# Optimization experiments

Hardware: AMD Instinct MI355X
Metric: run time of the kernel (lower is better)

Reference implementation:

```python
import jax, jax.numpy as jnp
import numpy as np

D_MODEL = 256
D_STATE = 64
R_MIN, R_MAX, MAX_PHASE = 0.0, 1.0, 6.28


def setup_inputs() -> dict:
    key = jax.random.key(0)
    ks = jax.random.split(key, 8)
    u1 = jax.random.uniform(ks[0], (D_STATE,), dtype=jnp.float32)
    u2 = jax.random.uniform(ks[1], (D_STATE,), dtype=jnp.float32)
    nu_log = jnp.log(-0.5 * jnp.log(u1 * (R_MAX**2 - R_MIN**2) + R_MIN**2))
    theta_log = jnp.log(u2 * MAX_PHASE)
    sB = 1.0 / np.sqrt(2 * D_STATE)
    sC = 1.0 / np.sqrt(D_STATE)
    B_re = jax.random.normal(ks[2], (D_MODEL, D_STATE), dtype=jnp.float32) * sB
    B_im = jax.random.normal(ks[3], (D_MODEL, D_STATE), dtype=jnp.float32) * sB
    C_re = jax.random.normal(ks[4], (D_MODEL, D_STATE), dtype=jnp.float32) * sC
    C_im = jax.random.normal(ks[5], (D_MODEL, D_STATE), dtype=jnp.float32) * sC
    D = jax.random.normal(ks[6], (D_MODEL,), dtype=jnp.float32)
    x = jax.random.normal(ks[7], (4, 8192, D_MODEL), dtype=jnp.float32)
    return {"x": x, "nu_log": nu_log, "theta_log": theta_log,
            "B_re": B_re, "B_im": B_im, "C_re": C_re, "C_im": C_im, "D": D}


def reference(x, nu_log, theta_log, B_re, B_im, C_re, C_im, D):
    B, L, H = x.shape
    # diagonal transition: Lambda = exp(-exp(nu) + i*exp(theta)); Lambda^k = exp(k*log_lambda)
    log_lambda = -jnp.exp(nu_log) + 1j * jnp.exp(theta_log)          # (n,)
    k = jnp.arange(L, dtype=jnp.float32)
    Lambda_k = jnp.exp(k[:, None] * log_lambda[None, :])              # (L, n) complex
    CB = (C_re + 1j * C_im) * (B_re + 1j * B_im)                      # (H, n)
    kernels = jnp.einsum('hn,ln->hl', CB, Lambda_k).real              # (H, L)
    # FFT (causal, linear) convolution per channel
    n_fft = 2 * L
    x_f = jnp.fft.rfft(x, n=n_fft, axis=1)                            # (B, L+1, H)
    k_f = jnp.fft.rfft(kernels, n=n_fft, axis=1)                      # (H, L+1)
    y_f = x_f * k_f.T[None]                                           # (B, L+1, H)
    y = jnp.fft.irfft(y_f, n=n_fft, axis=1)[:, :L, :]
    return y + x * D[None, None, :]
```

## Files before the change

### kernel.cpp

```cpp
#include <hip/hip_runtime.h>
#include <hip/hip_bf16.h>

#define BB   4
#define LL   8192
#define HH   256
#define NN   64
#define NSEG 128
#define LSEG 64
#define YCS  258

typedef __attribute__((ext_vector_type(8))) short  short8;
typedef __attribute__((ext_vector_type(4))) float  float4v;
typedef __attribute__((ext_vector_type(4))) int    int4v;


__device__ __forceinline__ float ldF(const void* p, size_t i, int isbf) {
    return isbf ? __bfloat162float(((const __hip_bfloat16*)p)[i])
                : ((const float*)p)[i];
}

__device__ __forceinline__ unsigned int packbf(float re, float im) {
    __hip_bfloat16 hr = __float2bfloat16(re);
    __hip_bfloat16 hi = __float2bfloat16(im);
    return ((unsigned int)*(unsigned short*)&hi << 16)
         |  (unsigned int)*(unsigned short*)&hr;
}
__device__ __forceinline__ float unpkre(unsigned int u) {
    unsigned short s = (unsigned short)(u & 0xFFFFu);
    return __bfloat162float(*(__hip_bfloat16*)&s);
}
__device__ __forceinline__ float unpkim(unsigned int u) {
    unsigned short s = (unsigned short)(u >> 16);
    return __bfloat162float(*(__hip_bfloat16*)&s);
}

__global__ void k_sniff(const void* p0, const void* p1, const void* p2,
                        const void* p3, const void* p4, const void* p5,
                        const void* p6, const void* p7, int* flags)
{
    int t = threadIdx.x;
    if (t < 8) {
        const void* ps[8] = {p0, p1, p2, p3, p4, p5, p6, p7};
        const unsigned int* d = (const unsigned int*)ps[t];
        int nbf = 0, nrand = 0;
        #pragma unroll
        for (int i = 0; i < 32; ++i) {
            unsigned int lo = d[i] & 0xFFFFu;
            unsigned int e  = (lo >> 7) & 0xFFu;
            if (lo == 0u) {  }
            else if (e >= 90u && e <= 140u) nbf++;
            else nrand++;
        }
        flags[t] = (nrand == 0 && nbf >= 8) ? 1 : 0;
    }
}

__global__ __launch_bounds__(256) void k_setup(
    const void* nu_log, const void* theta_log,
    const void* B_re, const void* B_im,
    const void* C_re, const void* C_im,
    const void* D, const int* __restrict__ flags,
    float* lam, float* lam64, float* Df, float* CBt,
    float* PsegRe, float* PsegIm)
{
    int t = blockIdx.x * 256 + threadIdx.x;
    if (t < NN) {
        float nu = expf(ldF(nu_log, t, flags[1]));
        float th = expf(ldF(theta_log, t, flags[2]));
        float a  = expf(-nu);
        lam[2*t]   = a * cosf(th);
        lam[2*t+1] = a * sinf(th);
        float a64 = expf(-64.0f * nu);
        float ph  = 64.0f * th;
        lam64[2*t]   = a64 * cosf(ph);
        lam64[2*t+1] = a64 * sinf(ph);
    }
    if (t < HH) Df[t] = ldF(D, t, flags[7]);
    if (t < HH * NN) {
        int h = t >> 6, n = t & 63;
        float bre = ldF(B_re, h*NN+n, flags[3]);
        float bim = ldF(B_im, h*NN+n, flags[4]);
        float cre = ldF(C_re, h*NN+n, flags[5]);
        float cim = ldF(C_im, h*NN+n, flags[6]);
        CBt[(n*2+0)*HH + h] = cre*bre - cim*bim;
        CBt[(n*2+1)*HH + h] = cre*bim + cim*bre;
    }
    if (t < 64 * 64) {
        int l = t >> 6, n = t & 63;
        float nu = expf(ldF(nu_log, n, flags[1]));
        float th = expf(ldF(theta_log, n, flags[2]));
        float fp = (float)(63 - l);
        float ar = expf(-fp * nu);
        PsegRe[t] = ar * cosf(fp * th);
        PsegIm[t] = ar * sinf(fp * th);
    }
}

__global__ __launch_bounds__(256) void k_ktab(
    const float* __restrict__ CBt, const float* __restrict__ PsegRe,
    const float* __restrict__ PsegIm, const float* __restrict__ lam64,
    float* __restrict__ Ktab,
    short* __restrict__ VreT, short* __restrict__ VimnT,
    short* __restrict__ PreH, short* __restrict__ PreL,
    short* __restrict__ PimH, short* __restrict__ PimL)
{
    int t = blockIdx.x * 256 + threadIdx.x;
    int h = t >> 6, j = t & 63;
    float acc = 0.f;
    for (int n = 0; n < NN; ++n)
        acc += CBt[(2*n)*HH + h]   * PsegRe[(63-j)*64 + n]
             - CBt[(2*n+1)*HH + h] * PsegIm[(63-j)*64 + n];
    Ktab[j*HH + h] = acc;
    if (t < 64*64) {
        int tau = t >> 6, n = t & 63;
        float vr, vi;
        if (tau < 63) {
            vr =  PsegRe[(62-tau)*64 + n];
            vi = -PsegIm[(62-tau)*64 + n];
        } else {
            vr =  lam64[2*n];
            vi = -lam64[2*n+1];
        }
        __hip_bfloat16 br = __float2bfloat16(vr);
        __hip_bfloat16 bi = __float2bfloat16(vi);
        VreT[tau*64 + n]  = *(short*)&br;
        VimnT[tau*64 + n] = *(short*)&bi;

        int n2 = t >> 6, l2 = t & 63;
        float pr = PsegRe[l2*64 + n2];
        float pi = PsegIm[l2*64 + n2];
        __hip_bfloat16 prh = __float2bfloat16(pr);
        __hip_bfloat16 prl = __float2bfloat16(pr - __bfloat162float(prh));
        __hip_bfloat16 pih = __float2bfloat16(pi);
        __hip_bfloat16 pil = __float2bfloat16(pi - __bfloat162float(pih));
        PreH[t] = *(short*)&prh;
        PreL[t] = *(short*)&prl;
        PimH[t] = *(short*)&pih;
        PimL[t] = *(short*)&pil;
    }
}

template<bool ISBF>
__device__ __forceinline__ void segsum_body(
    const void* __restrict__ x, size_t sb, unsigned int* __restrict__ xsh,
    const short* __restrict__ PreH, const short* __restrict__ PreL,
    const short* __restrict__ PimH, const short* __restrict__ PimL,
    unsigned int* __restrict__ Apack, size_t abase, int w, int q, int l15)
{
    int t = threadIdx.x;
    if (ISBF) {
        const short8* xp = (const short8*)((const short*)x + sb);
        #pragma unroll
        for (int i = 0; i < 8; ++i) {
            short8 v = xp[i*256 + t];
            int e = (i*256 + t) * 8;
            #pragma unroll
            for (int k = 0; k < 8; ++k)
                xsh[e + k] = (unsigned int)(unsigned short)v[k];
        }
    } else {
        const float4v* xp = (const float4v*)((const float*)x + sb);
        #pragma unroll
        for (int i = 0; i < 16; ++i) {
            float4v v = xp[i*256 + t];
            int e = (i*256 + t) * 4;
            #pragma unroll
            for (int k = 0; k < 4; ++k) {
                float xf = v[k];
                __hip_bfloat16 hv = __float2bfloat16(xf);
                __hip_bfloat16 lv = __float2bfloat16(xf - __bfloat162float(hv));
                xsh[e + k] = ((unsigned int)*(unsigned short*)&lv << 16)
                           |  (unsigned int)*(unsigned short*)&hv;
            }
        }
    }
    __syncthreads();

    #pragma unroll
    for (int nt = 0; nt < 4; ++nt) {
        short8 xh[2], xl[2];
        #pragma unroll
        for (int ks = 0; ks < 2; ++ks)
            #pragma unroll
            for (int j = 0; j < 8; ++j) {
                unsigned int u = xsh[(ks*32 + q*8 + j)*256 + w*64 + nt*16 + l15];
                xh[ks][j] = (short)(u & 0xFFFFu);
                if (!ISBF) xl[ks][j] = (short)(u >> 16);
            }
        #pragma unroll
        for (int mt = 0; mt < 4; ++mt) {
            float4v ar = {0.f, 0.f, 0.f, 0.f};
            float4v ai = {0.f, 0.f, 0.f, 0.f};
            #pragma unroll
            for (int ks = 0; ks < 2; ++ks) {
                int off = (mt*16 + l15)*64 + ks*32 + q*8;
                short8 prh = *(const short8*)(PreH + off);
                short8 pih = *(const short8*)(PimH + off);
                short8 prl = *(const short8*)(PreL + off);
                short8 pil = *(const short8*)(PimL + off);
                ar = __builtin_amdgcn_mfma_f32_16x16x32_bf16(prh, xh[ks], ar, 0, 0, 0);
                ai = __builtin_amdgcn_mfma_f32_16x16x32_bf16(pih, xh[ks], ai, 0, 0, 0);
                ar = __builtin_amdgcn_mfma_f32_16x16x32_bf16(prl, xh[ks], ar, 0, 0, 0);
                ai = __builtin_amdgcn_mfma_f32_16x16x32_bf16(pil, xh[ks], ai, 0, 0, 0);
                if (!ISBF) {
                    ar = __builtin_amdgcn_mfma_f32_16x16x32_bf16(prh, xl[ks], ar, 0, 0, 0);
                    ai = __builtin_amdgcn_mfma_f32_16x16x32_bf16(pih, xl[ks], ai, 0, 0, 0);
                }
            }
            #pragma unroll
            for (int r = 0; r < 4; ++r) {
                int n = mt*16 + q*4 + r;
                Apack[abase + (size_t)n*64 + nt*16 + l15] = packbf(ar[r], ai[r]);
            }
        }
    }
}

__global__ __launch_bounds__(256) void k_segsum(
    const void* __restrict__ x,
    const short* __restrict__ PreH, const short* __restrict__ PreL,
    const short* __restrict__ PimH, const short* __restrict__ PimL,
    const int* __restrict__ flags, unsigned int* __restrict__ Apack)
{
    __shared__ unsigned int xsh[64 * 256];
    int bk = blockIdx.x;
    int s  = bk & (NSEG - 1);
    int b  = bk >> 7;
    int w    = threadIdx.x >> 6;
    int lane = threadIdx.x & 63;
    int q = lane >> 4, l15 = lane & 15;

    size_t sb    = ((size_t)(b*LL) + s*64) * HH;
    size_t abase = (((size_t)(b*4 + w) * NSEG + s) * NN) * 64;

    if (flags[0]) segsum_body<true >(x, sb, xsh, PreH, PreL, PimH, PimL, Apack, abase, w, q, l15);
    else          segsum_body<false>(x, sb, xsh, PreH, PreL, PimH, PimL, Apack, abase, w, q, l15);
}

__global__ __launch_bounds__(256) void k_scan(
    const float* __restrict__ lam64, const float* __restrict__ CBt,
    unsigned int* __restrict__ Apack)
{
    int w    = blockIdx.x * 4 + (threadIdx.x >> 6);
    int lane = threadIdx.x & 63;
    int n    = w & 63;
    int hg   = (w >> 6) & 3;
    int b    = w >> 8;
    int h    = hg*64 + lane;

    float lre = lam64[2*n], lim = lam64[2*n+1];
    float cbre = CBt[(2*n)*HH + h], cbim = CBt[(2*n+1)*HH + h];
    float sre = 0.f, sim = 0.f;
    size_t base0 = (((size_t)(b*4 + hg) * NSEG) * NN + n) * 64 + lane;

    unsigned int curU[16], nxtU[16];
    #pragma unroll
    for (int k = 0; k < 16; ++k)
        curU[k] = Apack[base0 + (size_t)k * NN * 64];
    #pragma unroll
    for (int blk = 0; blk < 8; ++blk) {
        if (blk < 7) {
            #pragma unroll
            for (int k = 0; k < 16; ++k)
                nxtU[k] = Apack[base0 + (size_t)((blk+1)*16 + k) * NN * 64];
        }
        #pragma unroll
        for (int k = 0; k < 16; ++k) {
            size_t idx = base0 + (size_t)(blk*16 + k) * NN * 64;
            float are = unpkre(curU[k]);
            float aim = unpkim(curU[k]);
            float ure = cbre*sre - cbim*sim;
            float uim = cbre*sim + cbim*sre;
            Apack[idx] = packbf(ure, uim);
            float t2 = fmaf(lre, sre, fmaf(-lim, sim, are));
            sim = fmaf(lre, sim, fmaf(lim, sre, aim));
            sre = t2;
        }
        #pragma unroll
        for (int k = 0; k < 16; ++k) curU[k] = nxtU[k];
    }
}

template<bool ISBF, int U>
__device__ __forceinline__ void conv_u(
    const void* __restrict__ x, const float* __restrict__ Df,
    const float* __restrict__ Ktab, const short* __restrict__ xs,
    const float* __restrict__ yc,
    int b, int s, int h, float* __restrict__ y)
{
    int g0 = s*64 + U*16;
    size_t rbase = ((size_t)b*LL + g0)*HH + h;
    float xv[16], yv[16];
    float dh = Df[h];
    #pragma unroll
    for (int t = 0; t < 16; ++t) {
        float xl;
        if (ISBF) xl = __bfloat162float(((const __hip_bfloat16*)x)[rbase + (size_t)t*HH]);
        else      xl = ((const float*)x)[rbase + (size_t)t*HH];
        xv[t] = xl;
        yv[t] = fmaf(dh, xl, yc[(U*16 + t)*YCS + h]);
    }
    float kreg[16*U + 16];
    #pragma unroll
    for (int j = 0; j < 16*U + 16; ++j) kreg[j] = Ktab[j*HH + h];
    #pragma unroll
    for (int j = 0; j < 16; ++j)
        #pragma unroll
        for (int t = j; t < 16; ++t) yv[t] = fmaf(kreg[j], xv[t-j], yv[t]);
    #pragma unroll
    for (int m = 0; m < 16*U; ++m) {
        short bits = xs[(U*16 - 1 - m)*HH + h];
        float xm = __bfloat162float(*(const __hip_bfloat16*)&bits);
        #pragma unroll
        for (int t = 0; t < 16; ++t) yv[t] = fmaf(kreg[t+1+m], xm, yv[t]);
    }
    #pragma unroll
    for (int t = 0; t < 16; ++t) y[rbase + (size_t)t*HH] = yv[t];
}

template<bool ISBF>
__device__ __forceinline__ void cc_body(
    const short* __restrict__ VreT, const short* __restrict__ VimnT,
    const unsigned int* __restrict__ Upack, const void* __restrict__ x,
    const float* __restrict__ Df, const float* __restrict__ Ktab,
    float* yc, short* xs, int b, int s, float* __restrict__ y)
{
    int t = threadIdx.x;

    size_t sb = ((size_t)b*LL + s*64) * HH;
    if (ISBF) {
        const int4v* xp = (const int4v*)((const __hip_bfloat16*)x + sb);
        int4v* xd = (int4v*)xs;
        xd[t]        = xp[t];
        xd[t + 1024] = xp[t + 1024];
    } else {
        const float* xp = (const float*)x + sb;
        #pragma unroll
        for (int i = 0; i < 2; ++i) {
            int e = (t + i*1024) * 8;
            #pragma unroll
            for (int j = 0; j < 8; ++j) {
                __hip_bfloat16 v = __float2bfloat16(xp[e + j]);
                xs[e + j] = *(short*)&v;
            }
        }
    }

    int w = t >> 6, lane = t & 63;
    int hg = w & 3, nt = w >> 2;
    int q = lane >> 4, l15 = lane & 15;
    size_t ubase = (((size_t)(b*4 + hg) * NSEG + s) * NN) * 64;

    int l = nt*16 + l15;
    short8 bre[2], bim[2];
    #pragma unroll
    for (int ks = 0; ks < 2; ++ks)
        #pragma unroll
        for (int j = 0; j < 8; ++j) {
            int n = ks*32 + q*8 + j;
            unsigned int u = Upack[ubase + (size_t)n*64 + l];
            bre[ks][j] = (short)(u & 0xFFFFu);
            bim[ks][j] = (short)(u >> 16);
        }
    int h = hg*64 + l;
    #pragma unroll
    for (int mt = 0; mt < 4; ++mt) {
        float4v acc = {0.f, 0.f, 0.f, 0.f};
        #pragma unroll
        for (int ks = 0; ks < 2; ++ks) {
            int off = (mt*16 + l15)*64 + ks*32 + q*8;
            short8 afr = *(const short8*)(VreT + off);
            short8 afi = *(const short8*)(VimnT + off);
            acc = __builtin_amdgcn_mfma_f32_16x16x32_bf16(afr, bre[ks], acc, 0, 0, 0);
            acc = __builtin_amdgcn_mfma_f32_16x16x32_bf16(afi, bim[ks], acc, 0, 0, 0);
        }
        #pragma unroll
        for (int r = 0; r < 4; ++r) {
            int tau = mt*16 + q*4 + r;
            yc[tau*YCS + h] = acc[r];
        }
    }

    __syncthreads();

    int u = w >> 2;
    int h2 = hg*64 + lane;
    switch (u) {
        case 0: conv_u<ISBF,0>(x, Df, Ktab, xs, yc, b, s, h2, y); break;
        case 1: conv_u<ISBF,1>(x, Df, Ktab, xs, yc, b, s, h2, y); break;
        case 2: conv_u<ISBF,2>(x, Df, Ktab, xs, yc, b, s, h2, y); break;
        case 3: conv_u<ISBF,3>(x, Df, Ktab, xs, yc, b, s, h2, y); break;
    }
}

__global__ __launch_bounds__(1024) void k_cc(
    const short* __restrict__ VreT, const short* __restrict__ VimnT,
    const unsigned int* __restrict__ Upack, const void* __restrict__ x,
    const float* __restrict__ Df, const float* __restrict__ Ktab,
    const int* __restrict__ flags, float* __restrict__ y)
{
    __shared__ float yc[64 * YCS];
    __shared__ short xs[64 * HH];
    int bk = blockIdx.x;
    int s  = bk & (NSEG - 1);
    int b  = bk >> 7;
    if (flags[0]) cc_body<true >(VreT, VimnT, Upack, x, Df, Ktab, yc, xs, b, s, y);
    else          cc_body<false>(VreT, VimnT, Upack, x, Df, Ktab, yc, xs, b, s, y);
}

extern "C" void kernel_launch(void* const* d_in, const int* in_sizes, int n_in,
                              void* d_out, int out_size, void* d_ws, size_t ws_size,
                              hipStream_t stream)
{
    const void* x  = d_in[0];
    const void* nu = d_in[1];
    const void* th = d_in[2];
    const void* Br = d_in[3];
    const void* Bi = d_in[4];
    const void* Cr = d_in[5];
    const void* Ci = d_in[6];
    const void* D  = d_in[7];

    char* ws = (char*)d_ws;
    float* lam    = (float*)(ws);
    float* lam64  = (float*)(ws + 512);
    int*   flags  = (int*)(ws + 1024);
    float* Df     = (float*)(ws + 1088);
    float* CBt    = (float*)(ws + 2112);
    float* Ktab   = (float*)(ws + 133184);
    short* VreT   = (short*)(ws + 198720);
    short* VimnT  = (short*)(ws + 206912);
    float* PsegRe = (float*)(ws + 215104);
    float* PsegIm = (float*)(ws + 231744);
    short* PreH   = (short*)(ws + 248128);
    short* PreL   = (short*)(ws + 256320);
    short* PimH   = (short*)(ws + 264512);
    short* PimL   = (short*)(ws + 272704);
    unsigned int* Apack = (unsigned int*)(ws + 294912);
    float* yout = (float*)d_out;

    k_sniff<<<dim3(1), dim3(64), 0, stream>>>(x, nu, th, Br, Bi, Cr, Ci, D, flags);
    k_setup<<<dim3(64), dim3(256), 0, stream>>>(nu, th, Br, Bi, Cr, Ci, D, flags,
                                                lam, lam64, Df, CBt, PsegRe, PsegIm);
    k_ktab<<<dim3(64), dim3(256), 0, stream>>>(CBt, PsegRe, PsegIm, lam64,
                                               Ktab, VreT, VimnT,
                                               PreH, PreL, PimH, PimL);
    k_segsum<<<dim3(512), dim3(256), 0, stream>>>(x, PreH, PreL, PimH, PimL,
                                                  flags, Apack);
    k_scan<<<dim3(256), dim3(256), 0, stream>>>(lam64, CBt, Apack);
    k_cc<<<dim3(512), dim3(1024), 0, stream>>>(VreT, VimnT, Apack,
                                               x, Df, Ktab, flags, yout);
}
```

Baseline: 178.5 us.

## Fold dtype sniff into setup, deepen scan prefetch, drop LDS x staging

Removes the separate k_sniff launch by having each k_setup block detect input dtypes itself and block 0 publish the flags. The scan kernel now prefetches 32 segments per stage instead of 16, which raises register use. The conv stage no longer stages a bf16 copy of x in shared memory and instead reads earlier x values straight from global memory. For fp32 inputs this also keeps the history terms at full precision rather than rounding them to bf16. The trade-offs are more scattered global loads in the conv loop and extra registers in the scan.

```diff
diff --git a/kernel.cpp b/kernel.cpp
--- a/kernel.cpp
+++ b/kernel.cpp
@@ -19,6 +19,20 @@
                 : ((const float*)p)[i];
 }
 
+__device__ __forceinline__ int sniff1(const void* p) {
+    const unsigned int* d = (const unsigned int*)p;
+    int nbf = 0, nrand = 0;
+    #pragma unroll
+    for (int i = 0; i < 32; ++i) {
+        unsigned int lo = d[i] & 0xFFFFu;
+        unsigned int e  = (lo >> 7) & 0xFFu;
+        if (lo == 0u) {  }
+        else if (e >= 90u && e <= 140u) nbf++;
+        else nrand++;
+    }
+    return (nrand == 0 && nbf >= 8) ? 1 : 0;
+}
+
 __device__ __forceinline__ unsigned int packbf(float re, float im) {
     __hip_bfloat16 hr = __float2bfloat16(re);
     __hip_bfloat16 hi = __float2bfloat16(im);
@@ -34,39 +48,29 @@
     return __bfloat162float(*(__hip_bfloat16*)&s);
 }
 
-__global__ void k_sniff(const void* p0, const void* p1, const void* p2,
-                        const void* p3, const void* p4, const void* p5,
-                        const void* p6, const void* p7, int* flags)
-{
-    int t = threadIdx.x;
-    if (t < 8) {
-        const void* ps[8] = {p0, p1, p2, p3, p4, p5, p6, p7};
-        const unsigned int* d = (const unsigned int*)ps[t];
-        int nbf = 0, nrand = 0;
-        #pragma unroll
-        for (int i = 0; i < 32; ++i) {
-            unsigned int lo = d[i] & 0xFFFFu;
-            unsigned int e  = (lo >> 7) & 0xFFu;
-            if (lo == 0u) {  }
-            else if (e >= 90u && e <= 140u) nbf++;
-            else nrand++;
-        }
-        flags[t] = (nrand == 0 && nbf >= 8) ? 1 : 0;
-    }
-}
-
 __global__ __launch_bounds__(256) void k_setup(
-    const void* nu_log, const void* theta_log,
+    const void* x, const void* nu_log, const void* theta_log,
     const void* B_re, const void* B_im,
     const void* C_re, const void* C_im,
-    const void* D, const int* __restrict__ flags,
+    const void* D, int* flags,
     float* lam, float* lam64, float* Df, float* CBt,
     float* PsegRe, float* PsegIm)
 {
+    __shared__ int sf[8];
+    {
+        int tt = threadIdx.x;
+        if (tt < 8) {
+            const void* ps[8] = {x, nu_log, theta_log, B_re, B_im,
+                                 C_re, C_im, D};
+            sf[tt] = sniff1(ps[tt]);
+        }
+        __syncthreads();
+        if (blockIdx.x == 0 && tt < 8) flags[tt] = sf[tt];
+    }
     int t = blockIdx.x * 256 + threadIdx.x;
     if (t < NN) {
-        float nu = expf(ldF(nu_log, t, flags[1]));
-        float th = expf(ldF(theta_log, t, flags[2]));
+        float nu = expf(ldF(nu_log, t, sf[1]));
+        float th = expf(ldF(theta_log, t, sf[2]));
         float a  = expf(-nu);
         lam[2*t]   = a * cosf(th);
         lam[2*t+1] = a * sinf(th);
@@ -75,20 +79,20 @@
         lam64[2*t]   = a64 * cosf(ph);
         lam64[2*t+1] = a64 * sinf(ph);
     }
-    if (t < HH) Df[t] = ldF(D, t, flags[7]);
+    if (t < HH) Df[t] = ldF(D, t, sf[7]);
     if (t < HH * NN) {
         int h = t >> 6, n = t & 63;
-        float bre = ldF(B_re, h*NN+n, flags[3]);
-        float bim = ldF(B_im, h*NN+n, flags[4]);
-        float cre = ldF(C_re, h*NN+n, flags[5]);
-        float cim = ldF(C_im, h*NN+n, flags[6]);
+        float bre = ldF(B_re, h*NN+n, sf[3]);
+        float bim = ldF(B_im, h*NN+n, sf[4]);
+        float cre = ldF(C_re, h*NN+n, sf[5]);
+        float cim = ldF(C_im, h*NN+n, sf[6]);
         CBt[(n*2+0)*HH + h] = cre*bre - cim*bim;
         CBt[(n*2+1)*HH + h] = cre*bim + cim*bre;
     }
     if (t < 64 * 64) {
         int l = t >> 6, n = t & 63;
-        float nu = expf(ldF(nu_log, n, flags[1]));
-        float th = expf(ldF(theta_log, n, flags[2]));
+        float nu = expf(ldF(nu_log, n, sf[1]));
+        float th = expf(ldF(theta_log, n, sf[2]));
         float fp = (float)(63 - l);
         float ar = expf(-fp * nu);
         PsegRe[t] = ar * cosf(fp * th);
@@ -253,20 +257,20 @@
     float sre = 0.f, sim = 0.f;
     size_t base0 = (((size_t)(b*4 + hg) * NSEG) * NN + n) * 64 + lane;
 
-    unsigned int curU[16], nxtU[16];
-    #pragma unroll
-    for (int k = 0; k < 16; ++k)
+    unsigned int curU[32], nxtU[32];
+    #pragma unroll
+    for (int k = 0; k < 32; ++k)
         curU[k] = Apack[base0 + (size_t)k * NN * 64];
     #pragma unroll
-    for (int blk = 0; blk < 8; ++blk) {
-        if (blk < 7) {
-            #pragma unroll
-            for (int k = 0; k < 16; ++k)
-                nxtU[k] = Apack[base0 + (size_t)((blk+1)*16 + k) * NN * 64];
-        }
-        #pragma unroll
-        for (int k = 0; k < 16; ++k) {
-            size_t idx = base0 + (size_t)(blk*16 + k) * NN * 64;
+    for (int blk = 0; blk < 4; ++blk) {
+        if (blk < 3) {
+            #pragma unroll
+            for (int k = 0; k < 32; ++k)
+                nxtU[k] = Apack[base0 + (size_t)((blk+1)*32 + k) * NN * 64];
+        }
+        #pragma unroll
+        for (int k = 0; k < 32; ++k) {
+            size_t idx = base0 + (size_t)(blk*32 + k) * NN * 64;
             float are = unpkre(curU[k]);
             float aim = unpkim(curU[k]);
             float ure = cbre*sre - cbim*sim;
@@ -277,15 +281,14 @@
             sre = t2;
         }
         #pragma unroll
-        for (int k = 0; k < 16; ++k) curU[k] = nxtU[k];
+        for (int k = 0; k < 32; ++k) curU[k] = nxtU[k];
     }
 }
 
 template<bool ISBF, int U>
 __device__ __forceinline__ void conv_u(
     const void* __restrict__ x, const float* __restrict__ Df,
-    const float* __restrict__ Ktab, const short* __restrict__ xs,
-    const float* __restrict__ yc,
+    const float* __restrict__ Ktab, const float* __restrict__ yc,
     int b, int s, int h, float* __restrict__ y)
 {
     int g0 = s*64 + U*16;
@@ -309,8 +312,10 @@
         for (int t = j; t < 16; ++t) yv[t] = fmaf(kreg[j], xv[t-j], yv[t]);
     #pragma unroll
     for (int m = 0; m < 16*U; ++m) {
-        short bits = xs[(U*16 - 1 - m)*HH + h];
-        float xm = __bfloat162float(*(const __hip_bfloat16*)&bits);
+        float xm;
+        size_t ra = ((size_t)b*LL + (g0 - 1 - m))*HH + h;
+        if (ISBF) xm = __bfloat162float(((const __hip_bfloat16*)x)[ra]);
+        else      xm = ((const float*)x)[ra];
         #pragma unroll
         for (int t = 0; t < 16; ++t) yv[t] = fmaf(kreg[t+1+m], xm, yv[t]);
     }
@@ -323,28 +328,9 @@
     const short* __restrict__ VreT, const short* __restrict__ VimnT,
     const unsigned int* __restrict__ Upack, const void* __restrict__ x,
     const float* __restrict__ Df, const float* __restrict__ Ktab,
-    float* yc, short* xs, int b, int s, float* __restrict__ y)
+    float* yc, int b, int s, float* __restrict__ y)
 {
     int t = threadIdx.x;
-
-    size_t sb = ((size_t)b*LL + s*64) * HH;
-    if (ISBF) {
-        const int4v* xp = (const int4v*)((const __hip_bfloat16*)x + sb);
-        int4v* xd = (int4v*)xs;
-        xd[t]        = xp[t];
-        xd[t + 1024] = xp[t + 1024];
-    } else {
-        const float* xp = (const float*)x + sb;
-        #pragma unroll
-        for (int i = 0; i < 2; ++i) {
-            int e = (t + i*1024) * 8;
-            #pragma unroll
-            for (int j = 0; j < 8; ++j) {
-                __hip_bfloat16 v = __float2bfloat16(xp[e + j]);
-                xs[e + j] = *(short*)&v;
-            }
-        }
-    }
 
     int w = t >> 6, lane = t & 63;
     int hg = w & 3, nt = w >> 2;
@@ -386,10 +372,10 @@
     int u = w >> 2;
     int h2 = hg*64 + lane;
     switch (u) {
-        case 0: conv_u<ISBF,0>(x, Df, Ktab, xs, yc, b, s, h2, y); break;
-        case 1: conv_u<ISBF,1>(x, Df, Ktab, xs, yc, b, s, h2, y); break;
-        case 2: conv_u<ISBF,2>(x, Df, Ktab, xs, yc, b, s, h2, y); break;
-        case 3: conv_u<ISBF,3>(x, Df, Ktab, xs, yc, b, s, h2, y); break;
+        case 0: conv_u<ISBF,0>(x, Df, Ktab, yc, b, s, h2, y); break;
+        case 1: conv_u<ISBF,1>(x, Df, Ktab, yc, b, s, h2, y); break;
+        case 2: conv_u<ISBF,2>(x, Df, Ktab, yc, b, s, h2, y); break;
+        case 3: conv_u<ISBF,3>(x, Df, Ktab, yc, b, s, h2, y); break;
     }
 }
 
@@ -400,12 +386,11 @@
     const int* __restrict__ flags, float* __restrict__ y)
 {
     __shared__ float yc[64 * YCS];
-    __shared__ short xs[64 * HH];
     int bk = blockIdx.x;
     int s  = bk & (NSEG - 1);
     int b  = bk >> 7;
-    if (flags[0]) cc_body<true >(VreT, VimnT, Upack, x, Df, Ktab, yc, xs, b, s, y);
-    else          cc_body<false>(VreT, VimnT, Upack, x, Df, Ktab, yc, xs, b, s, y);
+    if (flags[0]) cc_body<true >(VreT, VimnT, Upack, x, Df, Ktab, yc, b, s, y);
+    else          cc_body<false>(VreT, VimnT, Upack, x, Df, Ktab, yc, b, s, y);
 }
 
 extern "C" void kernel_launch(void* const* d_in, const int* in_sizes, int n_in,
@@ -439,9 +424,9 @@
     unsigned int* Apack = (unsigned int*)(ws + 294912);
     float* yout = (float*)d_out;
 
-    k_sniff<<<dim3(1), dim3(64), 0, stream>>>(x, nu, th, Br, Bi, Cr, Ci, D, flags);
-    k_setup<<<dim3(64), dim3(256), 0, stream>>>(nu, th, Br, Bi, Cr, Ci, D, flags,
-                                                lam, lam64, Df, CBt, PsegRe, PsegIm);
+    k_setup<<<dim3(64), dim3(256), 0, stream>>>(x, nu, th, Br, Bi, Cr, Ci, D,
+                                                flags, lam, lam64, Df, CBt,
+                                                PsegRe, PsegIm);
     k_ktab<<<dim3(64), dim3(256), 0, stream>>>(CBt, PsegRe, PsegIm, lam64,
                                                Ktab, VreT, VimnT,
                                                PreH, PreL, PimH, PimL);
```

Result: no change. 176.4 us (median of 2 runs) (-1.1%).
